# Optimization experiments

Hardware: AMD Instinct MI355X
Metric: run time of the kernel (lower is better)

The kernel has to match this reference:

```python
import jax, jax.numpy as jnp
import numpy as np

P = 1  # scoring_norm (L1 distance, no GEMM shortcut)

def _lp_norm(v, p):
    # torch.norm(v, p=p, dim=-1)
    if p == 1:
        return jnp.sum(jnp.abs(v), axis=-1)
    return jnp.sum(jnp.abs(v) ** p, axis=-1) ** (1.0 / p)

def setup_inputs() -> dict:
    key = jax.random.key(0)
    k1, k2, k3, k4 = jax.random.split(key, 4)
    batch, n_neg, d, n_rel = 512, 2048, 128, 1000
    return {
        "head_emb": jax.random.normal(k1, (batch, d), dtype=jnp.float32),
        "relation_id": jax.random.randint(k2, (batch,), 0, n_rel, dtype=jnp.int64),
        "tail_emb": jax.random.normal(k3, (1, n_neg, d), dtype=jnp.float32),
        "relation_embedding": jax.random.normal(k4, (n_rel, d), dtype=jnp.float32),
    }

def reference(head_emb, relation_id, tail_emb, relation_embedding):
    # TransE.score_tails with negative_sample_sharing=True
    d = head_emb.shape[-1]
    rel = relation_embedding[relation_id]            # (batch, d)
    v1 = head_emb + rel                              # (batch, d) query
    v2 = tail_emb.reshape(-1, d)                     # (B*n_neg, d)
    diff = v1[:, None, :] - v2[None, :, :]           # (batch, B*n_neg, d)
    return -_lp_norm(diff, P)                        # (batch, B*n_neg)
```

## Files before the change

### kernel.cpp

```cpp
#include <hip/hip_runtime.h>

#define BATCH 512
#define NNEG  2048
#define DIM   128
#define TB    32
#define TN    64
#define PADR  132


__global__ __launch_bounds__(256)
void transe_l1_kernel(const float* __restrict__ head,
                      const int*   __restrict__ relid,
                      const float* __restrict__ tail,
                      const float* __restrict__ relemb,
                      float* __restrict__ out) {
    __shared__ float ltail[TN * PADR];
    __shared__ float lq[TB * PADR];

    const int tid   = threadIdx.x;
    const int bx    = blockIdx.x;
    const int ttile = bx & 31;
    const int btile = bx >> 5;
    const int t0    = ttile * TN;
    const int b0    = btile * TB;

    #pragma unroll
    for (int m = 0; m < 4; ++m) {
        int k   = tid + m * 256;
        int row = k >> 5;
        int c4  = k & 31;
        int b   = b0 + row;
        int rid = relid[b];
        float4 h = *reinterpret_cast<const float4*>(&head[b * DIM + c4 * 4]);
        float4 r = *reinterpret_cast<const float4*>(&relemb[rid * DIM + c4 * 4]);
        float4 q;
        q.x = h.x + r.x; q.y = h.y + r.y; q.z = h.z + r.z; q.w = h.w + r.w;
        *reinterpret_cast<float4*>(&lq[row * PADR + c4 * 4]) = q;
    }

    #pragma unroll
    for (int m = 0; m < 8; ++m) {
        int k   = tid + m * 256;
        int row = k >> 5;
        int c4  = k & 31;
        float4 tv = *reinterpret_cast<const float4*>(&tail[(t0 + row) * DIM + c4 * 4]);
        *reinterpret_cast<float4*>(&ltail[row * PADR + c4 * 4]) = tv;
    }

    __syncthreads();

    const int ts = tid & 7;
    const int bs = tid >> 3;

    float4 q[32];
    #pragma unroll
    for (int j = 0; j < 32; ++j) {
        q[j] = *reinterpret_cast<const float4*>(&lq[bs * PADR + j * 4]);
    }

    float res[8];
    #pragma unroll
    for (int i = 0; i < 8; ++i) {
        const float* tr = &ltail[(i * 8 + ts) * PADR];
        float sx = 0.f, sy = 0.f, sz = 0.f, sw = 0.f;
        #pragma unroll
        for (int j = 0; j < 32; ++j) {
            float4 tv = *reinterpret_cast<const float4*>(&tr[j * 4]);
            sx += fabsf(q[j].x - tv.x);
            sy += fabsf(q[j].y - tv.y);
            sz += fabsf(q[j].z - tv.z);
            sw += fabsf(q[j].w - tv.w);
        }
        res[i] = -((sx + sy) + (sz + sw));
    }

    const int b = b0 + bs;
    #pragma unroll
    for (int i = 0; i < 8; ++i) {
        out[b * NNEG + t0 + i * 8 + ts] = res[i];
    }
}

extern "C" void kernel_launch(void* const* d_in, const int* in_sizes, int n_in,
                              void* d_out, int out_size, void* d_ws, size_t ws_size,
                              hipStream_t stream) {
    const float* head   = (const float*)d_in[0];
    const int*   relid  = (const int*)d_in[1];
    const float* tail   = (const float*)d_in[2];
    const float* relemb = (const float*)d_in[3];
    float*       out    = (float*)d_out;

    dim3 grid((BATCH / TB) * (NNEG / TN));
    dim3 block(256);
    transe_l1_kernel<<<grid, block, 0, stream>>>(head, relid, tail, relemb, out);
}
```

Baseline: 15.55 us.

## Precompute queries in workspace and stream them via scalar loads

Splits the work into a small pre-kernel that computes head+relation queries into workspace and a main kernel. In the main kernel each lane keeps one tail row in registers, and the query rows, which are uniform across a wavefront, are streamed through SGPRs with double-buffered s_load_dwordx16 in inline asm. This removes the LDS query staging and the per-thread LDS reads of queries, since scalar operands feed the VALU directly. The cost is an extra kernel launch, a workspace round trip, and reliance on hand-written asm waitcnt ordering. A fallback path keeps the old kernel when the workspace is too small.

```diff
diff --git a/kernel.cpp b/kernel.cpp
--- a/kernel.cpp
+++ b/kernel.cpp
@@ -3,94 +3,179 @@
 #define BATCH 512
 #define NNEG  2048
 #define DIM   128
-#define TB    32
-#define TN    64
 #define PADR  132
 
+typedef int s16x __attribute__((ext_vector_type(16)));
+
+#define SLOAD2(r0, r1, p) \
+  asm volatile("s_load_dwordx16 %0, %2, 0x0\n\t" \
+               "s_load_dwordx16 %1, %2, 0x40" \
+               : "=s"(r0), "=s"(r1) : "s"(p))
+
+#define SWAIT2(r0, r1) \
+  asm volatile("s_waitcnt lgkmcnt(0)" : "+s"(r0), "+s"(r1))
+
+__device__ __forceinline__ void chunk32(const s16x& a0, const s16x& a1,
+                                        const float4* tr,
+                                        float& sx, float& sy, float& sz, float& sw) {
+#pragma unroll
+  for (int u = 0; u < 4; ++u) {
+    float4 t = tr[u];
+    sx += fabsf(__int_as_float(a0[4*u+0]) - t.x);
+    sy += fabsf(__int_as_float(a0[4*u+1]) - t.y);
+    sz += fabsf(__int_as_float(a0[4*u+2]) - t.z);
+    sw += fabsf(__int_as_float(a0[4*u+3]) - t.w);
+  }
+#pragma unroll
+  for (int u = 0; u < 4; ++u) {
+    float4 t = tr[u+4];
+    sx += fabsf(__int_as_float(a1[4*u+0]) - t.x);
+    sy += fabsf(__int_as_float(a1[4*u+1]) - t.y);
+    sz += fabsf(__int_as_float(a1[4*u+2]) - t.z);
+    sw += fabsf(__int_as_float(a1[4*u+3]) - t.w);
+  }
+}
 
 __global__ __launch_bounds__(256)
-void transe_l1_kernel(const float* __restrict__ head,
-                      const int*   __restrict__ relid,
-                      const float* __restrict__ tail,
-                      const float* __restrict__ relemb,
-                      float* __restrict__ out) {
-    __shared__ float ltail[TN * PADR];
-    __shared__ float lq[TB * PADR];
+void compute_q(const float* __restrict__ head, const int* __restrict__ relid,
+               const float* __restrict__ relemb, float* __restrict__ q) {
+  int i  = blockIdx.x * 256 + threadIdx.x;
+  int b  = i >> 5, c4 = i & 31;
+  int rid = relid[b];
+  float4 h = *reinterpret_cast<const float4*>(&head[b * DIM + c4 * 4]);
+  float4 r = *reinterpret_cast<const float4*>(&relemb[rid * DIM + c4 * 4]);
+  float4 o;
+  o.x = h.x + r.x; o.y = h.y + r.y; o.z = h.z + r.z; o.w = h.w + r.w;
+  *reinterpret_cast<float4*>(&q[b * DIM + c4 * 4]) = o;
+}
 
-    const int tid   = threadIdx.x;
-    const int bx    = blockIdx.x;
-    const int ttile = bx & 31;
-    const int btile = bx >> 5;
-    const int t0    = ttile * TN;
-    const int b0    = btile * TB;
+__global__ __launch_bounds__(256, 2)
+void transe_main(const float* __restrict__ tail, const float* __restrict__ q,
+                 float* __restrict__ out) {
+  __shared__ float lt[64 * PADR];
 
-    #pragma unroll
-    for (int m = 0; m < 4; ++m) {
-        int k   = tid + m * 256;
-        int row = k >> 5;
-        int c4  = k & 31;
-        int b   = b0 + row;
-        int rid = relid[b];
-        float4 h = *reinterpret_cast<const float4*>(&head[b * DIM + c4 * 4]);
-        float4 r = *reinterpret_cast<const float4*>(&relemb[rid * DIM + c4 * 4]);
-        float4 q;
-        q.x = h.x + r.x; q.y = h.y + r.y; q.z = h.z + r.z; q.w = h.w + r.w;
-        *reinterpret_cast<float4*>(&lq[row * PADR + c4 * 4]) = q;
+  const int tid = threadIdx.x;
+  const int bx  = blockIdx.x;
+  const int tt  = bx & 31;
+  const int bg  = bx >> 5;
+  const int t0  = tt * 64;
+  const int b0  = bg * 32;
+
+#pragma unroll
+  for (int m = 0; m < 8; ++m) {
+    int k = tid + m * 256;
+    int row = k >> 5, c4 = k & 31;
+    float4 v = *reinterpret_cast<const float4*>(&tail[(t0 + row) * DIM + c4 * 4]);
+    *reinterpret_cast<float4*>(&lt[row * PADR + c4 * 4]) = v;
+  }
+  __syncthreads();
+
+  const int lane = tid & 63;
+  const int wq   = __builtin_amdgcn_readfirstlane(tid >> 6);
+  const float* qb = q + (b0 + wq * 8) * DIM;
+
+  s16x A0, A1, B0, B1;
+  SLOAD2(A0, A1, qb);
+
+  float4 tr[32];
+#pragma unroll
+  for (int j = 0; j < 32; ++j)
+    tr[j] = *reinterpret_cast<const float4*>(&lt[lane * PADR + j * 4]);
+
+  SWAIT2(A0, A1);
+
+  float res[8];
+  float sx, sy, sz, sw;
+
+#define STEP(C0, C1, N0, N1, c)                                         \
+  do {                                                                  \
+    if ((c) < 31) { SLOAD2(N0, N1, qb + ((c) + 1) * 32); }              \
+    const int rr_ = (c) >> 2, s4_ = (c) & 3;                            \
+    if (s4_ == 0) { sx = sy = sz = sw = 0.f; }                          \
+    chunk32(C0, C1, &tr[8 * s4_], sx, sy, sz, sw);                      \
+    if (s4_ == 3) res[rr_] = -((sx + sy) + (sz + sw));                  \
+    if ((c) < 31) { SWAIT2(N0, N1); }                                   \
+  } while (0)
+
+  STEP(A0,A1,B0,B1, 0); STEP(B0,B1,A0,A1, 1); STEP(A0,A1,B0,B1, 2); STEP(B0,B1,A0,A1, 3);
+  STEP(A0,A1,B0,B1, 4); STEP(B0,B1,A0,A1, 5); STEP(A0,A1,B0,B1, 6); STEP(B0,B1,A0,A1, 7);
+  STEP(A0,A1,B0,B1, 8); STEP(B0,B1,A0,A1, 9); STEP(A0,A1,B0,B1,10); STEP(B0,B1,A0,A1,11);
+  STEP(A0,A1,B0,B1,12); STEP(B0,B1,A0,A1,13); STEP(A0,A1,B0,B1,14); STEP(B0,B1,A0,A1,15);
+  STEP(A0,A1,B0,B1,16); STEP(B0,B1,A0,A1,17); STEP(A0,A1,B0,B1,18); STEP(B0,B1,A0,A1,19);
+  STEP(A0,A1,B0,B1,20); STEP(B0,B1,A0,A1,21); STEP(A0,A1,B0,B1,22); STEP(B0,B1,A0,A1,23);
+  STEP(A0,A1,B0,B1,24); STEP(B0,B1,A0,A1,25); STEP(A0,A1,B0,B1,26); STEP(B0,B1,A0,A1,27);
+  STEP(A0,A1,B0,B1,28); STEP(B0,B1,A0,A1,29); STEP(A0,A1,B0,B1,30); STEP(B0,B1,A0,A1,31);
+#undef STEP
+
+  const int brow = b0 + wq * 8;
+#pragma unroll
+  for (int r = 0; r < 8; ++r)
+    out[(size_t)(brow + r) * NNEG + t0 + lane] = res[r];
+}
+
+__global__ __launch_bounds__(256)
+void transe_l1_fallback(const float* __restrict__ head, const int* __restrict__ relid,
+                        const float* __restrict__ tail, const float* __restrict__ relemb,
+                        float* __restrict__ out) {
+  __shared__ float ltail[64 * PADR];
+  __shared__ float lq[32 * PADR];
+  const int tid = threadIdx.x, bx = blockIdx.x;
+  const int t0 = (bx & 31) * 64, b0 = (bx >> 5) * 32;
+#pragma unroll
+  for (int m = 0; m < 4; ++m) {
+    int k = tid + m * 256, row = k >> 5, c4 = k & 31, b = b0 + row;
+    int rid = relid[b];
+    float4 h = *reinterpret_cast<const float4*>(&head[b * DIM + c4 * 4]);
+    float4 r = *reinterpret_cast<const float4*>(&relemb[rid * DIM + c4 * 4]);
+    float4 qv; qv.x=h.x+r.x; qv.y=h.y+r.y; qv.z=h.z+r.z; qv.w=h.w+r.w;
+    *reinterpret_cast<float4*>(&lq[row * PADR + c4 * 4]) = qv;
+  }
+#pragma unroll
+  for (int m = 0; m < 8; ++m) {
+    int k = tid + m * 256, row = k >> 5, c4 = k & 31;
+    float4 tv = *reinterpret_cast<const float4*>(&tail[(t0 + row) * DIM + c4 * 4]);
+    *reinterpret_cast<float4*>(&ltail[row * PADR + c4 * 4]) = tv;
+  }
+  __syncthreads();
+  const int ts = tid & 7, bs = tid >> 3;
+  float4 qv[32];
+#pragma unroll
+  for (int j = 0; j < 32; ++j)
+    qv[j] = *reinterpret_cast<const float4*>(&lq[bs * PADR + j * 4]);
+  float res[8];
+#pragma unroll
+  for (int i = 0; i < 8; ++i) {
+    const float* trp = &ltail[(i * 8 + ts) * PADR];
+    float sx = 0.f, sy = 0.f, sz = 0.f, sw = 0.f;
+#pragma unroll
+    for (int j = 0; j < 32; ++j) {
+      float4 tv = *reinterpret_cast<const float4*>(&trp[j * 4]);
+      sx += fabsf(qv[j].x - tv.x); sy += fabsf(qv[j].y - tv.y);
+      sz += fabsf(qv[j].z - tv.z); sw += fabsf(qv[j].w - tv.w);
     }
-
-    #pragma unroll
-    for (int m = 0; m < 8; ++m) {
-        int k   = tid + m * 256;
-        int row = k >> 5;
-        int c4  = k & 31;
-        float4 tv = *reinterpret_cast<const float4*>(&tail[(t0 + row) * DIM + c4 * 4]);
-        *reinterpret_cast<float4*>(&ltail[row * PADR + c4 * 4]) = tv;
-    }
-
-    __syncthreads();
-
-    const int ts = tid & 7;
-    const int bs = tid >> 3;
-
-    float4 q[32];
-    #pragma unroll
-    for (int j = 0; j < 32; ++j) {
-        q[j] = *reinterpret_cast<const float4*>(&lq[bs * PADR + j * 4]);
-    }
-
-    float res[8];
-    #pragma unroll
-    for (int i = 0; i < 8; ++i) {
-        const float* tr = &ltail[(i * 8 + ts) * PADR];
-        float sx = 0.f, sy = 0.f, sz = 0.f, sw = 0.f;
-        #pragma unroll
-        for (int j = 0; j < 32; ++j) {
-            float4 tv = *reinterpret_cast<const float4*>(&tr[j * 4]);
-            sx += fabsf(q[j].x - tv.x);
-            sy += fabsf(q[j].y - tv.y);
-            sz += fabsf(q[j].z - tv.z);
-            sw += fabsf(q[j].w - tv.w);
-        }
-        res[i] = -((sx + sy) + (sz + sw));
-    }
-
-    const int b = b0 + bs;
-    #pragma unroll
-    for (int i = 0; i < 8; ++i) {
-        out[b * NNEG + t0 + i * 8 + ts] = res[i];
-    }
+    res[i] = -((sx + sy) + (sz + sw));
+  }
+  const int b = b0 + bs;
+#pragma unroll
+  for (int i = 0; i < 8; ++i)
+    out[b * NNEG + t0 + i * 8 + ts] = res[i];
 }
 
 extern "C" void kernel_launch(void* const* d_in, const int* in_sizes, int n_in,
                               void* d_out, int out_size, void* d_ws, size_t ws_size,
                               hipStream_t stream) {
-    const float* head   = (const float*)d_in[0];
-    const int*   relid  = (const int*)d_in[1];
-    const float* tail   = (const float*)d_in[2];
-    const float* relemb = (const float*)d_in[3];
-    float*       out    = (float*)d_out;
+  const float* head   = (const float*)d_in[0];
+  const int*   relid  = (const int*)d_in[1];
+  const float* tail   = (const float*)d_in[2];
+  const float* relemb = (const float*)d_in[3];
+  float*       out    = (float*)d_out;
 
-    dim3 grid((BATCH / TB) * (NNEG / TN));
-    dim3 block(256);
-    transe_l1_kernel<<<grid, block, 0, stream>>>(head, relid, tail, relemb, out);
+  const size_t q_bytes = (size_t)BATCH * DIM * sizeof(float);
+  if (ws_size >= q_bytes) {
+    float* q = (float*)d_ws;
+    compute_q<<<dim3(BATCH * DIM / 4 / 256), dim3(256), 0, stream>>>(head, relid, relemb, q);
+    transe_main<<<dim3(32 * 16), dim3(256), 0, stream>>>(tail, q, out);
+  } else {
+    transe_l1_fallback<<<dim3(512), dim3(256), 0, stream>>>(head, relid, tail, relemb, out);
+  }
 }
```

Result: slower. 24.88 us (+60.1%).

## Split feature dimension across lanes with register-cached tail tile and shuffle reduction

Applied to the files above, without the earlier changes.

Each thread now caches a slice of eight tail rows in registers (a 16-float chunk of the feature dimension per row) and sweeps eight query rows. This replaces holding a full 128-wide query vector per thread and re-reading the whole tail row from LDS for every output. Partial L1 sums across the eight feature slices are combined with a butterfly of cross-lane xor shuffles that also transposes outputs to lanes. LDS uses XOR swizzling and a permuted query layout instead of padding to avoid bank conflicts. The change cuts LDS reads per FLOP and adds shuffle and select overhead plus high register pressure (tf alone is 128 VGPRs, with launch_bounds requesting 2 blocks/CU).

```diff
diff --git a/kernel.cpp b/kernel.cpp
--- a/kernel.cpp
+++ b/kernel.cpp
@@ -3,94 +3,118 @@
 #define BATCH 512
 #define NNEG  2048
 #define DIM   128
-#define TB    32
-#define TN    64
-#define PADR  132
 
 
-__global__ __launch_bounds__(256)
-void transe_l1_kernel(const float* __restrict__ head,
-                      const int*   __restrict__ relid,
-                      const float* __restrict__ tail,
-                      const float* __restrict__ relemb,
-                      float* __restrict__ out) {
-    __shared__ float ltail[TN * PADR];
-    __shared__ float lq[TB * PADR];
+__global__ __launch_bounds__(256, 2)
+void transe_l1(const float* __restrict__ head,
+               const int*   __restrict__ relid,
+               const float* __restrict__ tailp,
+               const float* __restrict__ relemb,
+               float* __restrict__ out) {
+  __shared__ float lds[96 * 128];
+  float* lt = lds;
+  float* lq = lds + 64 * 128;
 
-    const int tid   = threadIdx.x;
-    const int bx    = blockIdx.x;
-    const int ttile = bx & 31;
-    const int btile = bx >> 5;
-    const int t0    = ttile * TN;
-    const int b0    = btile * TB;
+  const int tid = threadIdx.x;
+  const int bx  = blockIdx.x;
+  const int t0  = (bx & 31) * 64;
+  const int b0  = (bx >> 5) * 32;
 
-    #pragma unroll
-    for (int m = 0; m < 4; ++m) {
-        int k   = tid + m * 256;
-        int row = k >> 5;
-        int c4  = k & 31;
-        int b   = b0 + row;
-        int rid = relid[b];
-        float4 h = *reinterpret_cast<const float4*>(&head[b * DIM + c4 * 4]);
-        float4 r = *reinterpret_cast<const float4*>(&relemb[rid * DIM + c4 * 4]);
-        float4 q;
-        q.x = h.x + r.x; q.y = h.y + r.y; q.z = h.z + r.z; q.w = h.w + r.w;
-        *reinterpret_cast<float4*>(&lq[row * PADR + c4 * 4]) = q;
+#pragma unroll
+  for (int m = 0; m < 8; ++m) {
+    int k = tid + m * 256;
+    int r = k >> 5, g = k & 31;
+    float4 v = *reinterpret_cast<const float4*>(&tailp[(t0 + r) * DIM + g * 4]);
+    int p = g ^ (r & 7);
+    *reinterpret_cast<float4*>(&lt[r * 128 + p * 4]) = v;
+  }
+#pragma unroll
+  for (int m = 0; m < 4; ++m) {
+    int k = tid + m * 256;
+    int r = k >> 5, g = k & 31;
+    int b = b0 + r;
+    int rid = relid[b];
+    float4 h = *reinterpret_cast<const float4*>(&head[b * DIM + g * 4]);
+    float4 e = *reinterpret_cast<const float4*>(&relemb[rid * DIM + g * 4]);
+    float4 v;
+    v.x = h.x + e.x; v.y = h.y + e.y; v.z = h.z + e.z; v.w = h.w + e.w;
+    int p = (g >> 2) + (g & 3) * 8;
+    *reinterpret_cast<float4*>(&lq[r * 128 + p * 4]) = v;
+  }
+  __syncthreads();
+
+  const int lane = tid & 63;
+  const int w    = tid >> 6;
+  const int tg   = lane & 7;
+  const int dg   = lane >> 3;
+
+  float4 tf[8][4];
+#pragma unroll
+  for (int k = 0; k < 8; ++k) {
+#pragma unroll
+    for (int j = 0; j < 4; ++j) {
+      int p = (dg * 4 + j) ^ tg;
+      tf[k][j] = *reinterpret_cast<const float4*>(&lt[(8 * k + tg) * 128 + p * 4]);
     }
+  }
 
-    #pragma unroll
-    for (int m = 0; m < 8; ++m) {
-        int k   = tid + m * 256;
-        int row = k >> 5;
-        int c4  = k & 31;
-        float4 tv = *reinterpret_cast<const float4*>(&tail[(t0 + row) * DIM + c4 * 4]);
-        *reinterpret_cast<float4*>(&ltail[row * PADR + c4 * 4]) = tv;
+  float acc[8][8];
+#pragma unroll
+  for (int r = 0; r < 8; ++r)
+#pragma unroll
+    for (int k = 0; k < 8; ++k) acc[r][k] = 0.f;
+
+  const int qbase = (w * 8) * 128;
+#pragma unroll
+  for (int r = 0; r < 8; ++r) {
+    float4 qf[4];
+#pragma unroll
+    for (int j = 0; j < 4; ++j)
+      qf[j] = *reinterpret_cast<const float4*>(&lq[qbase + r * 128 + (dg + 8 * j) * 4]);
+#pragma unroll
+    for (int k = 0; k < 8; ++k) {
+#pragma unroll
+      for (int j = 0; j < 4; ++j) {
+        acc[r][k] += fabsf(qf[j].x - tf[k][j].x);
+        acc[r][k] += fabsf(qf[j].y - tf[k][j].y);
+        acc[r][k] += fabsf(qf[j].z - tf[k][j].z);
+        acc[r][k] += fabsf(qf[j].w - tf[k][j].w);
+      }
     }
+  }
 
-    __syncthreads();
-
-    const int ts = tid & 7;
-    const int bs = tid >> 3;
-
-    float4 q[32];
-    #pragma unroll
-    for (int j = 0; j < 32; ++j) {
-        q[j] = *reinterpret_cast<const float4*>(&lq[bs * PADR + j * 4]);
+  const int brow = b0 + w * 8 + dg;
+#pragma unroll
+  for (int k = 0; k < 8; ++k) {
+    float s4[4];
+#pragma unroll
+    for (int i = 0; i < 4; ++i) {
+      float a  = acc[2 * i][k], b = acc[2 * i + 1][k];
+      float xa = __shfl_xor(a, 8), xb = __shfl_xor(b, 8);
+      s4[i] = (dg & 1) ? (b + xb) : (a + xa);
     }
-
-    float res[8];
-    #pragma unroll
-    for (int i = 0; i < 8; ++i) {
-        const float* tr = &ltail[(i * 8 + ts) * PADR];
-        float sx = 0.f, sy = 0.f, sz = 0.f, sw = 0.f;
-        #pragma unroll
-        for (int j = 0; j < 32; ++j) {
-            float4 tv = *reinterpret_cast<const float4*>(&tr[j * 4]);
-            sx += fabsf(q[j].x - tv.x);
-            sy += fabsf(q[j].y - tv.y);
-            sz += fabsf(q[j].z - tv.z);
-            sw += fabsf(q[j].w - tv.w);
-        }
-        res[i] = -((sx + sy) + (sz + sw));
+    float s2[2];
+#pragma unroll
+    for (int i = 0; i < 2; ++i) {
+      float a  = s4[2 * i], b = s4[2 * i + 1];
+      float xa = __shfl_xor(a, 16), xb = __shfl_xor(b, 16);
+      s2[i] = (dg & 2) ? (b + xb) : (a + xa);
     }
-
-    const int b = b0 + bs;
-    #pragma unroll
-    for (int i = 0; i < 8; ++i) {
-        out[b * NNEG + t0 + i * 8 + ts] = res[i];
-    }
+    float a  = s2[0], b = s2[1];
+    float xa = __shfl_xor(a, 32), xb = __shfl_xor(b, 32);
+    float v  = (dg & 4) ? (b + xb) : (a + xa);
+    out[brow * NNEG + t0 + 8 * k + tg] = -v;
+  }
 }
 
 extern "C" void kernel_launch(void* const* d_in, const int* in_sizes, int n_in,
                               void* d_out, int out_size, void* d_ws, size_t ws_size,
                               hipStream_t stream) {
-    const float* head   = (const float*)d_in[0];
-    const int*   relid  = (const int*)d_in[1];
-    const float* tail   = (const float*)d_in[2];
-    const float* relemb = (const float*)d_in[3];
-    float*       out    = (float*)d_out;
+  const float* head   = (const float*)d_in[0];
+  const int*   relid  = (const int*)d_in[1];
+  const float* tailp  = (const float*)d_in[2];
+  const float* relemb = (const float*)d_in[3];
+  float*       out    = (float*)d_out;
 
-    dim3 grid((BATCH / TB) * (NNEG / TN));
-    dim3 block(256);
-    transe_l1_kernel<<<grid, block, 0, stream>>>(head, relid, tail, relemb, out);
+  transe_l1<<<dim3(512), dim3(256), 0, stream>>>(head, relid, tailp, relemb, out);
 }
```

Result: faster. 15.05 us (-3.2%).
